# Optimization experiments

Measured on AMD Instinct MI355X. Metric: run time of the kernel, lower is better.

The kernel has to match this reference:

```python
import jax, jax.numpy as jnp
import numpy as np

B, N, IN_DIM, D, H, NC = 4, 1024, 8, 128, 8, 64
DK = D // H      # per-head key/value dim = 16
FF = 512         # hard-coded feedforward hidden
N_ENC = 6        # encoder layers


def _u(key, shape):
    s = 1.0 / np.sqrt(shape[-1])
    return jax.random.uniform(key, shape, jnp.float32, -s, s)


def setup_inputs() -> dict:
    key = jax.random.key(0)
    ks = jax.random.split(key, 24)
    inp = {}
    inp["node_inputs"] = jax.random.normal(ks[0], (B, N, IN_DIM), jnp.float32)
    inp["node_padding_mask"] = jnp.zeros((B, 1, N), jnp.int32)
    inp["edge_mask"] = jax.random.randint(ks[1], (B, N, N), 0, 2).astype(jnp.int32)
    inp["center_mask"] = jnp.zeros((B, 1, NC), jnp.int32)
    inp["center_index"] = jax.random.randint(ks[2], (B, 1, NC), 0, N)
    inp["target_index"] = jax.random.randint(ks[3], (B, 1, 1), 0, N)
    inp["current_index"] = jax.random.randint(ks[4], (B, 1, 1), 0, N)
    inp["edge_inputs"] = jax.random.randint(ks[5], (B, N, 20), 0, N)
    # params
    inp["init_W"] = _u(ks[6], (IN_DIM, D)); inp["init_b"] = jnp.zeros((D,), jnp.float32)
    inp["enc_wq"] = _u(ks[7], (N_ENC, H, D, DK))
    inp["enc_wk"] = _u(ks[8], (N_ENC, H, D, DK))
    inp["enc_wv"] = _u(ks[9], (N_ENC, H, D, DK))
    inp["enc_wo"] = _u(ks[10], (N_ENC, H, DK, D))
    inp["enc_ln1_g"] = jnp.ones((N_ENC, D), jnp.float32); inp["enc_ln1_b"] = jnp.zeros((N_ENC, D), jnp.float32)
    inp["enc_w1"] = _u(ks[11], (N_ENC, D, FF)); inp["enc_b1"] = jnp.zeros((N_ENC, FF), jnp.float32)
    inp["enc_w2"] = _u(ks[12], (N_ENC, FF, D)); inp["enc_b2"] = jnp.zeros((N_ENC, D), jnp.float32)
    inp["enc_ln2_g"] = jnp.ones((N_ENC, D), jnp.float32); inp["enc_ln2_b"] = jnp.zeros((N_ENC, D), jnp.float32)
    inp["dec_wq"] = _u(ks[13], (H, D, DK))
    inp["dec_wk"] = _u(ks[14], (H, D, DK))
    inp["dec_wv"] = _u(ks[15], (H, D, DK))
    inp["dec_wo"] = _u(ks[16], (H, DK, D))
    inp["dec_ln1_g"] = jnp.ones((D,), jnp.float32); inp["dec_ln1_b"] = jnp.zeros((D,), jnp.float32)
    inp["dec_w1"] = _u(ks[17], (D, FF)); inp["dec_b1"] = jnp.zeros((FF,), jnp.float32)
    inp["dec_w2"] = _u(ks[18], (FF, D)); inp["dec_b2"] = jnp.zeros((D,), jnp.float32)
    inp["dec_ln2_g"] = jnp.ones((D,), jnp.float32); inp["dec_ln2_b"] = jnp.zeros((D,), jnp.float32)
    inp["tgt_W"] = _u(ks[19], (2 * D, D)); inp["tgt_b"] = jnp.zeros((D,), jnp.float32)
    inp["ptr_wq"] = _u(ks[20], (D, D))
    inp["ptr_wk"] = _u(ks[21], (D, D))
    return inp


def _ln(x, g, b):
    m = jnp.mean(x, -1, keepdims=True)
    v = jnp.mean((x - m) ** 2, -1, keepdims=True)
    return (x - m) * jax.lax.rsqrt(v + 1e-5) * g + b


def _mha(q, k, v, wq, wk, wv, wo, mask):
    # per-head projections exactly as the torch module: [H, B, n, DK]
    Q = jnp.einsum('bqd,hde->hbqe', q, wq)
    K = jnp.einsum('bkd,hde->hbke', k, wk)
    V = jnp.einsum('bkd,hde->hbke', v, wv)
    U = jnp.einsum('hbqe,hbke->hbqk', Q, K) * (1.0 / np.sqrt(DK))
    if mask is not None:
        U = jnp.where(mask[None] > 0, -1e8, U)
    A = jax.nn.softmax(U, axis=-1)
    Hd = jnp.einsum('hbqk,hbke->hbqe', A, V)
    out = jnp.einsum('hbqe,hed->bqd', Hd, wo)
    return out, A


def _gather(x, idx):
    # x [B, N, D], idx [B, M, 1] -> [B, M, D]  (torch.gather with repeat)
    return jnp.take_along_axis(x, jnp.broadcast_to(idx, (x.shape[0], idx.shape[1], x.shape[2])), axis=1)


def reference(node_inputs, node_padding_mask, edge_mask, center_mask, center_index,
              target_index, current_index, edge_inputs,
              init_W, init_b,
              enc_wq, enc_wk, enc_wv, enc_wo, enc_ln1_g, enc_ln1_b,
              enc_w1, enc_b1, enc_w2, enc_b2, enc_ln2_g, enc_ln2_b,
              dec_wq, dec_wk, dec_wv, dec_wo, dec_ln1_g, dec_ln1_b,
              dec_w1, dec_b1, dec_w2, dec_b2, dec_ln2_g, dec_ln2_b,
              tgt_W, tgt_b, ptr_wq, ptr_wk):
    x = node_inputs @ init_W + init_b                      # initial_embedding
    enc_mask = edge_mask + node_padding_mask               # attn_mask + key_padding_mask, [B,N,N]
    for i in range(N_ENC):                                 # Encoder, 6 layers
        h = _ln(x, enc_ln1_g[i], enc_ln1_b[i])
        a, _ = _mha(h, h, h, enc_wq[i], enc_wk[i], enc_wv[i], enc_wo[i], enc_mask)
        h = a + x
        f = _ln(h, enc_ln2_g[i], enc_ln2_b[i])
        f = jax.nn.relu(f @ enc_w1[i] + enc_b1[i]) @ enc_w2[i] + enc_b2[i]
        x = f + h
    enh = x                                                # enhanced_node_feature [B,N,D]
    ci = jnp.transpose(center_index, (0, 2, 1))            # [B,NC,1]
    tgt_f = _gather(enh, target_index)                     # [B,1,D]
    cur_f = _gather(enh, current_index)                    # [B,1,D]
    cen_f = _gather(enh, ci)                               # [B,NC,D]
    # target_decoder (1 DecoderLayer; normalization1 applied to tgt AND memory)
    tgt_n = _ln(tgt_f, dec_ln1_g, dec_ln1_b)
    mem_n = _ln(enh, dec_ln1_g, dec_ln1_b)
    a, _ = _mha(tgt_n, mem_n, mem_n, dec_wq, dec_wk, dec_wv, dec_wo, node_padding_mask)
    h = a + tgt_f
    f = _ln(h, dec_ln2_g, dec_ln2_b)
    f = jax.nn.relu(f @ dec_w1 + dec_b1) @ dec_w2 + dec_b2
    enh_tgt = f + h                                        # [B,1,D]
    emb_tgt = jnp.concatenate([enh_tgt, tgt_f], -1) @ tgt_W + tgt_b
    # pointer1 (SingleHeadAttention, key_dim = D, tanh clipping 10)
    Q = emb_tgt @ ptr_wq                                   # [B,1,D]
    K = cen_f @ ptr_wk                                     # [B,NC,D]
    U = jnp.einsum('bqd,bkd->bqk', Q, K) * (1.0 / np.sqrt(D))
    U = 10.0 * jnp.tanh(U)
    U = jnp.where(center_mask == 1, -1e8, U)
    center_logp = jax.nn.log_softmax(U, axis=-1)[:, 0, :]  # [B,NC]
    idx = jnp.argmax(center_logp, axis=1)
    bidx = jnp.arange(B)
    selected_center_index = ci[bidx, idx, :]               # [B,1]
    selected_center_feature = cen_f[bidx, idx, :][:, None, :]  # [B,1,D]
    return (enh, cur_f, selected_center_index, selected_center_feature, center_logp, cen_f)
```

## Files before the change

### kernel.cpp

```cpp
#include <hip/hip_runtime.h>

constexpr int kB = 4, kN = 1024, kIn = 8, kD = 128, kH = 8, kNC = 64,
              kDK = 16, kFF = 512, kEnc = 6, kR = kB * kN;

__device__ __forceinline__ float wredsum(float v) {
  v += __shfl_xor(v, 1);  v += __shfl_xor(v, 2);  v += __shfl_xor(v, 4);
  v += __shfl_xor(v, 8);  v += __shfl_xor(v, 16); v += __shfl_xor(v, 32);
  return v;
}
__device__ __forceinline__ float wredmax(float v) {
  v = fmaxf(v, __shfl_xor(v, 1));  v = fmaxf(v, __shfl_xor(v, 2));
  v = fmaxf(v, __shfl_xor(v, 4));  v = fmaxf(v, __shfl_xor(v, 8));
  v = fmaxf(v, __shfl_xor(v, 16)); v = fmaxf(v, __shfl_xor(v, 32));
  return v;
}
__device__ __forceinline__ float red4(float v) {
  v += __shfl_xor(v, 1);  v += __shfl_xor(v, 2);
  return v;
}


__global__ __launch_bounds__(256) void repack_qkv(
    const float* __restrict__ wq, const float* __restrict__ wk,
    const float* __restrict__ wv, float* __restrict__ out, int layers) {
  int i = blockIdx.x * 256 + threadIdx.x;
  if (i >= layers * kD * kD) return;
  int l = i / (kD * kD);
  int rem = i - l * kD * kD;
  int d = rem >> 7;
  int c = rem & 127;
  int src = ((l * kH + (c >> 4)) * kD + d) * kDK + (c & 15);
  out[(size_t)(l * 3 + 0) * 16384 + rem] = wq[src];
  out[(size_t)(l * 3 + 1) * 16384 + rem] = wk[src];
  out[(size_t)(l * 3 + 2) * 16384 + rem] = wv[src];
}

__global__ __launch_bounds__(256) void pack_mask(
    const int* __restrict__ edge_mask, const int* __restrict__ pad_mask,
    unsigned long long* __restrict__ bits_t) {
  int row = blockIdx.x;
  int b = row / kN;
  int q = row % kN;
  int lane = threadIdx.x & 63;
  int wv = threadIdx.x >> 6;
  for (int c0 = wv; c0 < 16; c0 += 4) {
    int k = c0 * 64 + lane;
    int m = edge_mask[(size_t)row * kN + k] + pad_mask[b * kN + k];
    unsigned long long bal = __ballot(m > 0);
    if (lane == 0) bits_t[((size_t)b * 16 + c0) * kN + q] = bal;
  }
}

__global__ __launch_bounds__(256) void pack_pad(
    const int* __restrict__ pad_mask, unsigned long long* __restrict__ bits) {
  int b = blockIdx.x;
  int lane = threadIdx.x & 63;
  int wv = threadIdx.x >> 6;
  for (int c0 = wv; c0 < 16; c0 += 4) {
    int k = c0 * 64 + lane;
    unsigned long long bal = __ballot(pad_mask[b * kN + k] > 0);
    if (lane == 0) bits[b * 16 + c0] = bal;
  }
}

__global__ __launch_bounds__(256) void init_proj(
    const float* __restrict__ ni, const float* __restrict__ W,
    const float* __restrict__ bias, float* __restrict__ x) {
  int i = blockIdx.x * 256 + threadIdx.x;
  int r = i >> 7, c = i & 127;
  float acc = bias[c];
#pragma unroll
  for (int k = 0; k < kIn; k++) acc = fmaf(ni[r * kIn + k], W[k * kD + c], acc);
  x[i] = acc;
}

template <int K, int LN, int RELU, int MODE>
__global__ __launch_bounds__(256) void gtile4(
    const float* __restrict__ A, const float* __restrict__ Wg,
    const float* __restrict__ gamma, const float* __restrict__ beta,
    const float* __restrict__ bias, const float* __restrict__ resid,
    float* __restrict__ O0, float* __restrict__ O1, float* __restrict__ O2,
    int Cfull) {
  constexpr int NC = K / 32;
  __shared__ float As[16][K + 4];
  __shared__ float Ws[2][32][128];
  int r0 = blockIdx.x * 16;
  int y = blockIdx.y;
  const float* Wb;
  int wstride;
  if constexpr (MODE == 2) { Wb = Wg + (size_t)y * K * 128; wstride = 128; }
  else { Wb = Wg + (size_t)y * 128; wstride = Cfull; }

  if constexpr (LN) {
    static_assert(K == 128, "LN requires K==128");
    int w = threadIdx.x >> 6, lane = threadIdx.x & 63;
#pragma unroll
    for (int i = 0; i < 4; i++) {
      int rr = w * 4 + i;
      const float* xr = A + (size_t)(r0 + rr) * 128;
      float2 v = *(const float2*)(xr + lane * 2);
      float mean = wredsum(v.x + v.y) * (1.0f / 128.f);
      float dx = v.x - mean, dy = v.y - mean;
      float var = wredsum(dx * dx + dy * dy) * (1.0f / 128.f);
      float rstd = rsqrtf(var + 1e-5f);
      int c = lane * 2;
      As[rr][c] = dx * rstd * gamma[c] + beta[c];
      As[rr][c + 1] = dy * rstd * gamma[c + 1] + beta[c + 1];
    }
  } else {
    constexpr int NF4 = K / 4;
    for (int f = threadIdx.x; f < 16 * NF4; f += 256) {
      int row = f / NF4, c4i = f % NF4;
      *(float4*)&As[row][c4i * 4] =
          *(const float4*)(A + (size_t)(r0 + row) * K + c4i * 4);
    }
  }

  int wrow = threadIdx.x >> 5;
  int wc4 = threadIdx.x & 31;
  float4 wreg[4];
  auto loadW = [&](int kc) {
    const float* Wr = Wb + (size_t)(kc * 32 + wrow) * wstride + wc4 * 4;
#pragma unroll
    for (int j = 0; j < 4; j++)
      wreg[j] = *(const float4*)(Wr + (size_t)8 * j * wstride);
  };
  auto writeW = [&](int buf) {
#pragma unroll
    for (int j = 0; j < 4; j++)
      *(float4*)&Ws[buf][wrow + 8 * j][wc4 * 4] = wreg[j];
  };

  loadW(0);
  writeW(0);

  int c4 = (threadIdx.x & 31) * 4;
  int rg = threadIdx.x >> 5;
  float acc[2][4] = {};
  for (int kc = 0; kc < NC; kc++) {
    if (kc + 1 < NC) loadW(kc + 1);
    __syncthreads();
#pragma unroll
    for (int k4 = 0; k4 < 8; k4++) {
      float4 a0 = *(const float4*)&As[rg * 2][kc * 32 + k4 * 4];
      float4 a1 = *(const float4*)&As[rg * 2 + 1][kc * 32 + k4 * 4];
#pragma unroll
      for (int m = 0; m < 4; m++) {
        float4 wv = *(const float4*)&Ws[kc & 1][k4 * 4 + m][c4];
        float av0 = ((const float*)&a0)[m];
        float av1 = ((const float*)&a1)[m];
        acc[0][0] = fmaf(av0, wv.x, acc[0][0]);
        acc[0][1] = fmaf(av0, wv.y, acc[0][1]);
        acc[0][2] = fmaf(av0, wv.z, acc[0][2]);
        acc[0][3] = fmaf(av0, wv.w, acc[0][3]);
        acc[1][0] = fmaf(av1, wv.x, acc[1][0]);
        acc[1][1] = fmaf(av1, wv.y, acc[1][1]);
        acc[1][2] = fmaf(av1, wv.z, acc[1][2]);
        acc[1][3] = fmaf(av1, wv.w, acc[1][3]);
      }
    }
    if (kc + 1 < NC) writeW((kc + 1) & 1);
  }

#pragma unroll
  for (int rr = 0; rr < 2; rr++) {
    int r = r0 + rg * 2 + rr;
    if constexpr (MODE == 2) {
#pragma unroll
      for (int j = 0; j < 4; j++) {
        int c = c4 + j;
        float v = acc[rr][j];
        int hh = c >> 4, e = c & 15;
        int bb = r >> 10, n = r & 1023;
        float* P = (y == 0) ? O0 : (y == 1) ? O1 : O2;
        P[(((size_t)(bb * kH + hh)) * kN + n) * kDK + e] = v;
      }
    } else {
      int colg = y * 128 + c4;
      float4 v = make_float4(acc[rr][0], acc[rr][1], acc[rr][2], acc[rr][3]);
      if (bias) {
        float4 bv = *(const float4*)(bias + colg);
        v.x += bv.x; v.y += bv.y; v.z += bv.z; v.w += bv.w;
      }
      if (resid) {
        float4 rv = *(const float4*)(resid + (size_t)r * Cfull + colg);
        v.x += rv.x; v.y += rv.y; v.z += rv.z; v.w += rv.w;
      }
      if (RELU) {
        v.x = fmaxf(v.x, 0.f); v.y = fmaxf(v.y, 0.f);
        v.z = fmaxf(v.z, 0.f); v.w = fmaxf(v.w, 0.f);
      }
      *(float4*)(O0 + (size_t)r * Cfull + colg) = v;
    }
  }
}

__global__ __launch_bounds__(512) void attn_part(
    const float* __restrict__ Q, const float* __restrict__ K,
    const float* __restrict__ V, const unsigned long long* __restrict__ bits_t,
    float* __restrict__ part) {
  __shared__ float Ks[8][64][20];
  __shared__ float Vs[8][64][20];
  int bh = blockIdx.x, qt = blockIdx.y, ks = blockIdx.z;
  int b = bh >> 3;
  int w = threadIdx.x >> 6, lane = threadIdx.x & 63;
  int qbase = qt * 256 + lane;
  float4 qr[4][4];
#pragma unroll
  for (int i = 0; i < 4; i++) {
    const float4* qp = (const float4*)(Q + ((size_t)bh * kN + qbase + i * 64) * kDK);
    qr[i][0] = qp[0]; qr[i][1] = qp[1]; qr[i][2] = qp[2]; qr[i][3] = qp[3];
  }
  int kk = ks * 512 + w * 64 + lane;
  {
    const float4* kp = (const float4*)(K + ((size_t)bh * kN + kk) * kDK);
    const float4* vp = (const float4*)(V + ((size_t)bh * kN + kk) * kDK);
    ((float4*)&Ks[w][lane][0])[0] = kp[0]; ((float4*)&Ks[w][lane][0])[1] = kp[1];
    ((float4*)&Ks[w][lane][0])[2] = kp[2]; ((float4*)&Ks[w][lane][0])[3] = kp[3];
    ((float4*)&Vs[w][lane][0])[0] = vp[0]; ((float4*)&Vs[w][lane][0])[1] = vp[1];
    ((float4*)&Vs[w][lane][0])[2] = vp[2]; ((float4*)&Vs[w][lane][0])[3] = vp[3];
  }
  int tile = ks * 8 + w;
  unsigned long long mb[4];
#pragma unroll
  for (int i = 0; i < 4; i++)
    mb[i] = bits_t[((size_t)b * 16 + tile) * kN + qbase + i * 64];

  float mx[4], lsum[4], acc[4][16];
#pragma unroll
  for (int i = 0; i < 4; i++) {
    mx[i] = -3.0e38f; lsum[i] = 0.f;
#pragma unroll
    for (int e = 0; e < 16; e++) acc[i][e] = 0.f;
  }

#pragma unroll 2
  for (int k2 = 0; k2 < 64; k2++) {
    const float4* kr = (const float4*)&Ks[w][k2][0];
    float4 k0 = kr[0], k1 = kr[1], k2v = kr[2], k3 = kr[3];
    const float4* vr = (const float4*)&Vs[w][k2][0];
    float4 v0 = vr[0], v1 = vr[1], v2 = vr[2], v3 = vr[3];
#pragma unroll
    for (int i = 0; i < 4; i++) {
      float s = qr[i][0].x * k0.x + qr[i][0].y * k0.y + qr[i][0].z * k0.z +
                qr[i][0].w * k0.w + qr[i][1].x * k1.x + qr[i][1].y * k1.y +
                qr[i][1].z * k1.z + qr[i][1].w * k1.w + qr[i][2].x * k2v.x +
                qr[i][2].y * k2v.y + qr[i][2].z * k2v.z + qr[i][2].w * k2v.w +
                qr[i][3].x * k3.x + qr[i][3].y * k3.y + qr[i][3].z * k3.z +
                qr[i][3].w * k3.w;
      s *= 0.25f;
      if ((mb[i] >> k2) & 1ull) s = -1e8f;
      float d = s - mx[i];
      if (d > 8.f) {
        float sc = __expf(-d);
        lsum[i] *= sc;
#pragma unroll
        for (int e = 0; e < 16; e++) acc[i][e] *= sc;
        mx[i] = s; d = 0.f;
      }
      float p = __expf(d);
      lsum[i] += p;
      acc[i][0] = fmaf(p, v0.x, acc[i][0]);
      acc[i][1] = fmaf(p, v0.y, acc[i][1]);
      acc[i][2] = fmaf(p, v0.z, acc[i][2]);
      acc[i][3] = fmaf(p, v0.w, acc[i][3]);
      acc[i][4] = fmaf(p, v1.x, acc[i][4]);
      acc[i][5] = fmaf(p, v1.y, acc[i][5]);
      acc[i][6] = fmaf(p, v1.z, acc[i][6]);
      acc[i][7] = fmaf(p, v1.w, acc[i][7]);
      acc[i][8] = fmaf(p, v2.x, acc[i][8]);
      acc[i][9] = fmaf(p, v2.y, acc[i][9]);
      acc[i][10] = fmaf(p, v2.z, acc[i][10]);
      acc[i][11] = fmaf(p, v2.w, acc[i][11]);
      acc[i][12] = fmaf(p, v3.x, acc[i][12]);
      acc[i][13] = fmaf(p, v3.y, acc[i][13]);
      acc[i][14] = fmaf(p, v3.z, acc[i][14]);
      acc[i][15] = fmaf(p, v3.w, acc[i][15]);
    }
  }
  __syncthreads();
  for (int i = 0; i < 4; i++) {
    float* dst = &Ks[w][lane][0];
#pragma unroll
    for (int e = 0; e < 16; e++) dst[e] = acc[i][e];
    dst[16] = mx[i];
    dst[17] = lsum[i];
    __syncthreads();
    if (w == 0) {
      float mv[8];
#pragma unroll
      for (int p = 0; p < 8; p++) mv[p] = Ks[p][lane][16];
      float mstar = mv[0];
#pragma unroll
      for (int p = 1; p < 8; p++) mstar = fmaxf(mstar, mv[p]);
      float f[8];
      float L = 0.f;
#pragma unroll
      for (int p = 0; p < 8; p++) {
        f[p] = __expf(mv[p] - mstar);
        L += f[p] * Ks[p][lane][17];
      }
      int q = qt * 256 + i * 64 + lane;
      float* op = part + ((size_t)(ks * 32 + bh) * kN + q) * 20;
#pragma unroll
      for (int e = 0; e < 16; e++) {
        float a = 0.f;
#pragma unroll
        for (int p = 0; p < 8; p++) a += f[p] * Ks[p][lane][e];
        op[e] = a;
      }
      op[16] = mstar;
      op[17] = L;
    }
    __syncthreads();
  }
}

__global__ __launch_bounds__(256) void attn_merge(
    const float* __restrict__ part, float* __restrict__ Hd) {
  int idx = blockIdx.x * 256 + threadIdx.x;
  int bh = idx >> 10, q = idx & 1023;
  int b = bh >> 3, h = bh & 7;
  const float* p0 = part + ((size_t)(0 * 32 + bh) * kN + q) * 20;
  const float* p1 = part + ((size_t)(1 * 32 + bh) * kN + q) * 20;
  float m0 = p0[16], l0 = p0[17], m1 = p1[16], l1 = p1[17];
  float ms = fmaxf(m0, m1);
  float f0 = __expf(m0 - ms), f1 = __expf(m1 - ms);
  float inv = 1.0f / (f0 * l0 + f1 * l1);
  float* op = Hd + ((size_t)(b * kN + q)) * kD + h * kDK;
#pragma unroll
  for (int e = 0; e < 16; e++) op[e] = (f0 * p0[e] + f1 * p1[e]) * inv;
}


__global__ __launch_bounds__(256) void dec_prep(
    const float* __restrict__ enh, const int* __restrict__ tgt_idx,
    const int* __restrict__ cur_idx, const int* __restrict__ cen_idx,
    const float* __restrict__ Wq,
    const float* __restrict__ ln1_g, const float* __restrict__ ln1_b,
    const float* __restrict__ dec_wk,
    float* __restrict__ out_curf, float* __restrict__ out_cenf,
    float* __restrict__ tgtf_ws, float* __restrict__ qk_ws) {
  __shared__ float tgtf_s[128], tgtn[128], qd[128];
  int b = blockIdx.x, t = threadIdx.x;
  int lane = t & 63, w = t >> 6;
  int ti = tgt_idx[b], cui = cur_idx[b];
  if (t < 128) {
    float tf = enh[((size_t)b * kN + ti) * kD + t];
    tgtf_s[t] = tf;
    tgtf_ws[b * kD + t] = tf;
    out_curf[b * kD + t] = enh[((size_t)b * kN + cui) * kD + t];
  }
  for (int i = t; i < kNC * kD; i += 256) {
    int c = i >> 7, e = i & 127;
    out_cenf[((size_t)b * kNC + c) * kD + e] =
        enh[((size_t)b * kN + cen_idx[b * kNC + c]) * kD + e];
  }
  __syncthreads();
  if (w == 0) {
    float vx = tgtf_s[lane * 2], vy = tgtf_s[lane * 2 + 1];
    float mean = wredsum(vx + vy) * (1.0f / 128.f);
    float dx = vx - mean, dy = vy - mean;
    float var = wredsum(dx * dx + dy * dy) * (1.0f / 128.f);
    float rstd = rsqrtf(var + 1e-5f);
    tgtn[lane * 2] = dx * rstd * ln1_g[lane * 2] + ln1_b[lane * 2];
    tgtn[lane * 2 + 1] = dy * rstd * ln1_g[lane * 2 + 1] + ln1_b[lane * 2 + 1];
  }
  __syncthreads();
  if (t < 128) {
    float a = 0.f;
#pragma unroll 8
    for (int k = 0; k < 128; k++) a = fmaf(tgtn[k], Wq[k * 128 + t], a);
    qd[t] = a;
  }
  __syncthreads();
  int h = t >> 5, d0 = (t & 31) * 4;
#pragma unroll
  for (int j = 0; j < 4; j++) {
    int d = d0 + j;
    const float4* wp = (const float4*)(dec_wk + (((size_t)h * 128 + d) << 4));
    float a = 0.f;
#pragma unroll
    for (int r = 0; r < 4; r++) {
      float4 wv = wp[r];
      a += wv.x * qd[h * 16 + r * 4] + wv.y * qd[h * 16 + r * 4 + 1] +
           wv.z * qd[h * 16 + r * 4 + 2] + wv.w * qd[h * 16 + r * 4 + 3];
    }
    qk_ws[b * 1024 + h * 128 + d] = 0.25f * a;
  }
}

__global__ __launch_bounds__(256) void dec_score(
    const float* __restrict__ enh, const float* __restrict__ ln_g,
    const float* __restrict__ ln_b, const float* __restrict__ qk_ws,
    const unsigned long long* __restrict__ padbits,
    float* __restrict__ ln_ws, float* __restrict__ scores) {
  __shared__ float qs[8][128];
  int b = blockIdx.x, nt = blockIdx.y, t = threadIdx.x;
  for (int i = t; i < 1024; i += 256) ((float*)qs)[i] = qk_ws[b * 1024 + i];
  __syncthreads();
  int w = t >> 6, lane = t & 63, ri = lane >> 2, q4 = lane & 3;
  int n = nt * 64 + w * 16 + ri;
  const float* row = enh + ((size_t)b * kN + n) * kD;
  float4 xv[8];
#pragma unroll
  for (int j = 0; j < 8; j++) xv[j] = *(const float4*)(row + j * 16 + q4 * 4);
  float s1 = 0.f;
#pragma unroll
  for (int j = 0; j < 8; j++) s1 += xv[j].x + xv[j].y + xv[j].z + xv[j].w;
  s1 = red4(s1);
  float mean = s1 * (1.0f / 128.f);
  float s2 = 0.f;
#pragma unroll
  for (int j = 0; j < 8; j++) {
    xv[j].x -= mean; xv[j].y -= mean; xv[j].z -= mean; xv[j].w -= mean;
    s2 += xv[j].x * xv[j].x + xv[j].y * xv[j].y + xv[j].z * xv[j].z +
          xv[j].w * xv[j].w;
  }
  s2 = red4(s2);
  float rstd = rsqrtf(s2 * (1.0f / 128.f) + 1e-5f);
#pragma unroll
  for (int j = 0; j < 8; j++) {
    int d0 = j * 16 + q4 * 4;
    float4 g = *(const float4*)(ln_g + d0);
    float4 be = *(const float4*)(ln_b + d0);
    xv[j].x = xv[j].x * rstd * g.x + be.x;
    xv[j].y = xv[j].y * rstd * g.y + be.y;
    xv[j].z = xv[j].z * rstd * g.z + be.z;
    xv[j].w = xv[j].w * rstd * g.w + be.w;
    *(float4*)(ln_ws + ((size_t)b * kN + n) * kD + d0) = xv[j];
  }
  bool mk = (padbits[b * 16 + (n >> 6)] >> (n & 63)) & 1ull;
#pragma unroll
  for (int h = 0; h < 8; h++) {
    float p = 0.f;
#pragma unroll
    for (int j = 0; j < 8; j++) {
      float4 qv = *(const float4*)&qs[h][j * 16 + q4 * 4];
      p += xv[j].x * qv.x + xv[j].y * qv.y + xv[j].z * qv.z + xv[j].w * qv.w;
    }
    p = red4(p);
    if (q4 == 0) scores[((size_t)b * 8 + h) * 1024 + n] = mk ? -1e8f : p;
  }
}

__global__ __launch_bounds__(256) void dec_softmax(
    const float* __restrict__ scores, float* __restrict__ ml) {
  int b = blockIdx.x, t = threadIdx.x, w = t >> 6, lane = t & 63;
  for (int hi = 0; hi < 2; hi++) {
    int h = w + hi * 4;
    const float* sr = scores + ((size_t)b * 8 + h) * 1024;
    float v[16];
    float m = -3.0e38f;
#pragma unroll
    for (int i = 0; i < 16; i++) { v[i] = sr[i * 64 + lane]; m = fmaxf(m, v[i]); }
    m = wredmax(m);
    float l = 0.f;
#pragma unroll
    for (int i = 0; i < 16; i++) l += __expf(v[i] - m);
    l = wredsum(l);
    if (lane == 0) { ml[(b * 8 + h) * 2] = m; ml[(b * 8 + h) * 2 + 1] = l; }
  }
}

__global__ __launch_bounds__(256) void dec_attnsum(
    const float* __restrict__ ln_ws, const float* __restrict__ scores,
    const float* __restrict__ ml, float* __restrict__ partial) {
  __shared__ float lns[64][128];
  __shared__ float ps[8][64];
  int b = blockIdx.x, nt = blockIdx.y, t = threadIdx.x;
  for (int i = t; i < 64 * 32; i += 256) {
    int nn = i >> 5, c4 = i & 31;
    *(float4*)&lns[nn][c4 * 4] =
        *(const float4*)(ln_ws + ((size_t)b * kN + nt * 64 + nn) * kD + c4 * 4);
  }
  for (int i = t; i < 512; i += 256) {
    int h = i >> 6, nn = i & 63;
    float m = ml[(b * 8 + h) * 2], l = ml[(b * 8 + h) * 2 + 1];
    ps[h][nn] =
        __expf(scores[((size_t)b * 8 + h) * 1024 + nt * 64 + nn] - m) / l;
  }
  __syncthreads();
  int h = t >> 5, d0 = (t & 31) * 4;
  float4 acc = make_float4(0.f, 0.f, 0.f, 0.f);
  for (int nn = 0; nn < 64; nn++) {
    float p = ps[h][nn];
    float4 lv = *(const float4*)&lns[nn][d0];
    acc.x = fmaf(p, lv.x, acc.x); acc.y = fmaf(p, lv.y, acc.y);
    acc.z = fmaf(p, lv.z, acc.z); acc.w = fmaf(p, lv.w, acc.w);
  }
  *(float4*)(partial + ((size_t)(b * 16 + nt) * 8 + h) * 128 + d0) = acc;
}

__global__ __launch_bounds__(1024) void dec_tail(
    const float* __restrict__ partial, const float* __restrict__ dec_wv,
    const float* __restrict__ dwo, const float* __restrict__ tgtf_ws,
    const float* __restrict__ cenf_g, const float* __restrict__ Kp,
    const int* __restrict__ cen_idx, const int* __restrict__ center_mask,
    const float* __restrict__ ln2_g, const float* __restrict__ ln2_b,
    const float* __restrict__ w1, const float* __restrict__ b1,
    const float* __restrict__ w2, const float* __restrict__ b2,
    const float* __restrict__ tgt_W, const float* __restrict__ tgt_b,
    const float* __restrict__ ptr_wq,
    float* __restrict__ out_selidx, float* __restrict__ out_selfeat,
    float* __restrict__ out_logp) {
  __shared__ float wsum[8][132];
  __shared__ float red[8][132];
  __shared__ float red2[2][520];
  __shared__ float red16[16][68];
  __shared__ float tgtf[128], hdd[128], dechs[128], decfs[128], dects[512],
                   embs[128], qps[128];
  __shared__ int bi_s;
  int b = blockIdx.x, t = threadIdx.x;
  int c = t & 127, p = t >> 7;
  int lane = t & 63, w = t >> 6;

  {
    float a = 0.f;
#pragma unroll
    for (int tt = 0; tt < 16; tt++)
      a += partial[((size_t)(b * 16 + tt) * 8 + p) * 128 + c];
    wsum[p][c] = a;
    if (t < 128) tgtf[t] = tgtf_ws[b * kD + t];
  }
  __syncthreads();

  {
    int h = c >> 4, e = c & 15;
    float a = 0.f;
#pragma unroll
    for (int i = 0; i < 16; i++) {
      int d = p * 16 + i;
      a = fmaf(wsum[h][d], dec_wv[((size_t)h * 128 + d) * 16 + e], a);
    }
    red[p][c] = a;
  }
  __syncthreads();
  if (t < 128) {
    float a = 0.f;
#pragma unroll
    for (int q = 0; q < 8; q++) a += red[q][t];
    hdd[t] = a;
  }
  __syncthreads();

  {
    float a = 0.f;
#pragma unroll
    for (int i = 0; i < 16; i++) {
      int k = p * 16 + i;
      a = fmaf(hdd[k], dwo[k * 128 + c], a);
    }
    red[p][c] = a;
  }
  __syncthreads();
  if (t < 128) {
    float a = 0.f;
#pragma unroll
    for (int q = 0; q < 8; q++) a += red[q][t];
    dechs[t] = a + tgtf[t];
  }
  __syncthreads();

  if (w == 0) {
    float vx = dechs[lane * 2], vy = dechs[lane * 2 + 1];
    float mean = wredsum(vx + vy) * (1.0f / 128.f);
    float dx = vx - mean, dy = vy - mean;
    float var = wredsum(dx * dx + dy * dy) * (1.0f / 128.f);
    float rstd = rsqrtf(var + 1e-5f);
    decfs[lane * 2] = dx * rstd * ln2_g[lane * 2] + ln2_b[lane * 2];
    decfs[lane * 2 + 1] = dy * rstd * ln2_g[lane * 2 + 1] + ln2_b[lane * 2 + 1];
  }
  __syncthreads();

  {
    int c5 = t & 511, p2 = t >> 9;
    float a = 0.f;
#pragma unroll 8
    for (int i = 0; i < 64; i++) {
      int k = p2 * 64 + i;
      a = fmaf(decfs[k], w1[k * 512 + c5], a);
    }
    red2[p2][c5] = a;
  }
  __syncthreads();
  if (t < 512) dects[t] = fmaxf(red2[0][t] + red2[1][t] + b1[t], 0.f);
  __syncthreads();

  {
    float a = 0.f;
#pragma unroll 8
    for (int i = 0; i < 64; i++) {
      int k = p * 64 + i;
      a = fmaf(dects[k], w2[k * 128 + c], a);
    }
    red[p][c] = a;
  }
  __syncthreads();
  if (t < 128) {
    float a = 0.f;
#pragma unroll
    for (int q = 0; q < 8; q++) a += red[q][t];
    decfs[t] = a + b2[t] + dechs[t];
  }
  __syncthreads();

  {
    float a = 0.f;
#pragma unroll
    for (int i = 0; i < 32; i++) {
      int k = p * 32 + i;
      float vkk = (k < 128) ? decfs[k] : tgtf[k - 128];
      a = fmaf(vkk, tgt_W[k * 128 + c], a);
    }
    red[p][c] = a;
  }
  __syncthreads();
  if (t < 128) {
    float a = 0.f;
#pragma unroll
    for (int q = 0; q < 8; q++) a += red[q][t];
    embs[t] = a + tgt_b[t];
  }
  __syncthreads();

  {
    float a = 0.f;
#pragma unroll
    for (int i = 0; i < 16; i++) {
      int k = p * 16 + i;
      a = fmaf(embs[k], ptr_wq[k * 128 + c], a);
    }
    red[p][c] = a;
  }
  __syncthreads();
  if (t < 128) {
    float a = 0.f;
#pragma unroll
    for (int q = 0; q < 8; q++) a += red[q][t];
    qps[t] = a;
  }
  __syncthreads();

  {
    int cen = t & 63, p16 = t >> 6;
    float a = 0.f;
#pragma unroll
    for (int i = 0; i < 8; i++) {
      int k = p16 * 8 + i;
      a = fmaf(qps[k], Kp[((size_t)(b * kNC + cen)) * kD + k], a);
    }
    red16[p16][cen] = a;
  }
  __syncthreads();
  if (w == 0) {
    float u = 0.f;
#pragma unroll
    for (int q = 0; q < 16; q++) u += red16[q][lane];
    u *= 0.08838834764831845f;
    u = 10.0f * tanhf(u);
    if (center_mask[b * kNC + lane] == 1) u = -1e8f;
    float m = wredmax(u);
    float ex = __expf(u - m);
    float sum = wredsum(ex);
    out_logp[b * kNC + lane] = u - m - logf(sum);
    float bm = u; int bi = lane;
#pragma unroll
    for (int o = 32; o; o >>= 1) {
      float om = __shfl_xor(bm, o);
      int oi = __shfl_xor(bi, o);
      if (om > bm || (om == bm && oi < bi)) { bm = om; bi = oi; }
    }
    if (lane == 0) {
      out_selidx[b] = (float)cen_idx[b * kNC + bi];
      bi_s = bi;
    }
  }
  __syncthreads();
  if (t < 128)
    out_selfeat[b * kD + t] = cenf_g[((size_t)(b * kNC + bi_s)) * kD + t];
}


extern "C" void kernel_launch(void* const* d_in, const int* in_sizes, int n_in,
                              void* d_out, int out_size, void* d_ws,
                              size_t ws_size, hipStream_t stream) {
  (void)in_sizes; (void)n_in; (void)out_size; (void)ws_size;
  const float* node_inputs = (const float*)d_in[0];
  const int* pad_mask = (const int*)d_in[1];
  const int* edge_mask = (const int*)d_in[2];
  const int* center_mask = (const int*)d_in[3];
  const int* center_index = (const int*)d_in[4];
  const int* target_index = (const int*)d_in[5];
  const int* current_index = (const int*)d_in[6];
  const float* init_W = (const float*)d_in[8];
  const float* init_b = (const float*)d_in[9];
  const float* enc_wq = (const float*)d_in[10];
  const float* enc_wk = (const float*)d_in[11];
  const float* enc_wv = (const float*)d_in[12];
  const float* enc_wo = (const float*)d_in[13];
  const float* enc_ln1_g = (const float*)d_in[14];
  const float* enc_ln1_b = (const float*)d_in[15];
  const float* enc_w1 = (const float*)d_in[16];
  const float* enc_b1 = (const float*)d_in[17];
  const float* enc_w2 = (const float*)d_in[18];
  const float* enc_b2 = (const float*)d_in[19];
  const float* enc_ln2_g = (const float*)d_in[20];
  const float* enc_ln2_b = (const float*)d_in[21];
  const float* dec_wq = (const float*)d_in[22];
  const float* dec_wk = (const float*)d_in[23];
  const float* dec_wv = (const float*)d_in[24];
  const float* dec_wo = (const float*)d_in[25];
  const float* dec_ln1_g = (const float*)d_in[26];
  const float* dec_ln1_b = (const float*)d_in[27];
  const float* dec_w1 = (const float*)d_in[28];
  const float* dec_b1 = (const float*)d_in[29];
  const float* dec_w2 = (const float*)d_in[30];
  const float* dec_b2 = (const float*)d_in[31];
  const float* dec_ln2_g = (const float*)d_in[32];
  const float* dec_ln2_b = (const float*)d_in[33];
  const float* tgt_W = (const float*)d_in[34];
  const float* tgt_b = (const float*)d_in[35];
  const float* ptr_wq = (const float*)d_in[36];
  const float* ptr_wk = (const float*)d_in[37];

  float* out_enh = (float*)d_out;
  float* out_curf = out_enh + kB * kN * kD;
  float* out_selidx = out_curf + kB * kD;
  float* out_selfeat = out_selidx + kB;
  float* out_logp = out_selfeat + kB * kD;
  float* out_cenf = out_logp + kB * kNC;

  char* wsp = (char*)d_ws;
  size_t off = 0;
  auto alloc = [&](size_t n) {
    char* p = wsp + off;
    off = (off + n + 255) & ~(size_t)255;
    return p;
  };
  float* x   = (float*)alloc(kR * kD * 4);
  float* h2  = (float*)alloc(kR * kD * 4);
  float* Qb  = (float*)alloc(kR * kD * 4);
  float* Kb  = (float*)alloc(kR * kD * 4);
  float* Vb  = (float*)alloc(kR * kD * 4);
  float* Hd  = (float*)alloc(kR * kD * 4);
  float* tb  = (float*)alloc(kR * kFF * 4);
  unsigned long long* bits_t  = (unsigned long long*)alloc(kR * 16 * 8);
  unsigned long long* padbits = (unsigned long long*)alloc(kB * 16 * 8);
  float* ewqkv = (float*)alloc(kEnc * 3 * kD * kD * 4);
  float* dqkvW = (float*)alloc(3 * kD * kD * 4);
  float* ln_ws = (float*)alloc(kR * kD * 4);
  float* scores_ws = (float*)alloc(kB * kH * kN * 4);
  float* ml_ws = (float*)alloc(kB * kH * 2 * 4);
  float* partial_ws = (float*)alloc(kB * 16 * kH * kD * 4);
  float* qk_ws = (float*)alloc(kB * kH * kD * 4);
  float* tgtf_ws = (float*)alloc(kB * kD * 4);
  float* Kp_ws = (float*)alloc(kB * kNC * kD * 4);
  float* apart_ws = (float*)alloc((size_t)2 * 32 * kN * 20 * 4);

  repack_qkv<<<(kEnc * kD * kD + 255) / 256, 256, 0, stream>>>(
      enc_wq, enc_wk, enc_wv, ewqkv, kEnc);
  repack_qkv<<<(kD * kD + 255) / 256, 256, 0, stream>>>(
      dec_wq, dec_wk, dec_wv, dqkvW, 1);
  pack_mask<<<kB * kN, 256, 0, stream>>>(edge_mask, pad_mask, bits_t);
  pack_pad<<<kB, 256, 0, stream>>>(pad_mask, padbits);
  init_proj<<<kR * kD / 256, 256, 0, stream>>>(node_inputs, init_W, init_b, x);

  for (int l = 0; l < kEnc; l++) {
    const float* wo_l = enc_wo + (size_t)l * kH * kDK * kD;
    gtile4<128, 1, 0, 2><<<dim3(kR / 16, 3), 256, 0, stream>>>(
        x, ewqkv + (size_t)l * 3 * kD * kD, enc_ln1_g + l * kD,
        enc_ln1_b + l * kD, nullptr, nullptr, Qb, Kb, Vb, kD);
    attn_part<<<dim3(kB * kH, kN / 256, 2), 512, 0, stream>>>(Qb, Kb, Vb,
                                                              bits_t, apart_ws);
    attn_merge<<<(kB * kH * kN) / 256, 256, 0, stream>>>(apart_ws, Hd);
    gtile4<128, 0, 0, 0><<<dim3(kR / 16, 1), 256, 0, stream>>>(
        Hd, wo_l, nullptr, nullptr, nullptr, x, h2, nullptr, nullptr, kD);
    gtile4<128, 1, 1, 0><<<dim3(kR / 16, kFF / 128), 256, 0, stream>>>(
        h2, enc_w1 + (size_t)l * kD * kFF, enc_ln2_g + l * kD,
        enc_ln2_b + l * kD, enc_b1 + l * kFF, nullptr, tb, nullptr, nullptr, kFF);
    float* xout = (l == kEnc - 1) ? out_enh : x;
    gtile4<512, 0, 0, 0><<<dim3(kR / 16, 1), 256, 0, stream>>>(
        tb, enc_w2 + (size_t)l * kFF * kD, nullptr, nullptr, enc_b2 + l * kD,
        h2, xout, nullptr, nullptr, kD);
  }

  dec_prep<<<kB, 256, 0, stream>>>(out_enh, target_index, current_index,
                                   center_index, dqkvW, dec_ln1_g, dec_ln1_b,
                                   dec_wk, out_curf, out_cenf, tgtf_ws, qk_ws);
  gtile4<128, 0, 0, 0><<<dim3(kB * kNC / 16, 1), 256, 0, stream>>>(
      out_cenf, ptr_wk, nullptr, nullptr, nullptr, nullptr, Kp_ws, nullptr,
      nullptr, kD);
  dec_score<<<dim3(kB, 16), 256, 0, stream>>>(out_enh, dec_ln1_g, dec_ln1_b,
                                              qk_ws, padbits, ln_ws, scores_ws);
  dec_softmax<<<kB, 256, 0, stream>>>(scores_ws, ml_ws);
  dec_attnsum<<<dim3(kB, 16), 256, 0, stream>>>(ln_ws, scores_ws, ml_ws,
                                                partial_ws);
  dec_tail<<<kB, 1024, 0, stream>>>(
      partial_ws, dec_wv, dec_wo, tgtf_ws, out_cenf, Kp_ws, center_index,
      center_mask, dec_ln2_g, dec_ln2_b, dec_w1, dec_b1, dec_w2, dec_b2,
      tgt_W, tgt_b, ptr_wq, out_selidx, out_selfeat, out_logp);
}
```

Before: 824.6 us.

## Fuse attention split-merge into output projection GEMM and shrink attn LDS

Removes the separate attn_merge kernel and the Hd buffer by adding a MODE 3 A-loader to gtile4 that merges the two key-split partial softmax results directly while staging the A tile. Separately, attn_part now stages K/V through shared memory in two 32-row halves, roughly halving its LDS footprint so more blocks can be resident. This saves one launch per layer and a full write and read of the head output, at the cost of a heavier A-load in the projection GEMM with strided partial reads. The scratch reuse during the final reduction still fits the smaller buffer.

```diff
diff --git a/kernel.cpp b/kernel.cpp
--- a/kernel.cpp
+++ b/kernel.cpp
@@ -106,6 +106,28 @@
       int c = lane * 2;
       As[rr][c] = dx * rstd * gamma[c] + beta[c];
       As[rr][c + 1] = dy * rstd * gamma[c + 1] + beta[c + 1];
+    }
+  } else if constexpr (MODE == 3) {
+    static_assert(K == 128, "merge stage requires K==128");
+    for (int f = threadIdx.x; f < 16 * 32; f += 256) {
+      int row = f >> 5, c4i = f & 31;
+      int r = r0 + row;
+      int bb = r >> 10, q = r & 1023;
+      int hh = c4i >> 2, e4 = (c4i & 3) * 4;
+      const float* p0 = A + ((size_t)((bb * kH + hh) * kN + q)) * 20;
+      const float* p1 = p0 + (size_t)32 * kN * 20;
+      float m0 = p0[16], l0 = p0[17], m1 = p1[16], l1 = p1[17];
+      float ms = fmaxf(m0, m1);
+      float f0 = __expf(m0 - ms), f1 = __expf(m1 - ms);
+      float inv = 1.0f / (f0 * l0 + f1 * l1);
+      float4 a0 = *(const float4*)(p0 + e4);
+      float4 a1 = *(const float4*)(p1 + e4);
+      float4 o;
+      o.x = (f0 * a0.x + f1 * a1.x) * inv;
+      o.y = (f0 * a0.y + f1 * a1.y) * inv;
+      o.z = (f0 * a0.z + f1 * a1.z) * inv;
+      o.w = (f0 * a0.w + f1 * a1.w) * inv;
+      *(float4*)&As[row][c4i * 4] = o;
     }
   } else {
     constexpr int NF4 = K / 4;
@@ -199,8 +221,7 @@
     const float* __restrict__ Q, const float* __restrict__ K,
     const float* __restrict__ V, const unsigned long long* __restrict__ bits_t,
     float* __restrict__ part) {
-  __shared__ float Ks[8][64][20];
-  __shared__ float Vs[8][64][20];
+  __shared__ float KV[2][8][32][20];
   int bh = blockIdx.x, qt = blockIdx.y, ks = blockIdx.z;
   int b = bh >> 3;
   int w = threadIdx.x >> 6, lane = threadIdx.x & 63;
@@ -208,17 +229,9 @@
   float4 qr[4][4];
 #pragma unroll
   for (int i = 0; i < 4; i++) {
-    const float4* qp = (const float4*)(Q + ((size_t)bh * kN + qbase + i * 64) * kDK);
+    const float4* qp =
+        (const float4*)(Q + ((size_t)bh * kN + qbase + i * 64) * kDK);
     qr[i][0] = qp[0]; qr[i][1] = qp[1]; qr[i][2] = qp[2]; qr[i][3] = qp[3];
-  }
-  int kk = ks * 512 + w * 64 + lane;
-  {
-    const float4* kp = (const float4*)(K + ((size_t)bh * kN + kk) * kDK);
-    const float4* vp = (const float4*)(V + ((size_t)bh * kN + kk) * kDK);
-    ((float4*)&Ks[w][lane][0])[0] = kp[0]; ((float4*)&Ks[w][lane][0])[1] = kp[1];
-    ((float4*)&Ks[w][lane][0])[2] = kp[2]; ((float4*)&Ks[w][lane][0])[3] = kp[3];
-    ((float4*)&Vs[w][lane][0])[0] = vp[0]; ((float4*)&Vs[w][lane][0])[1] = vp[1];
-    ((float4*)&Vs[w][lane][0])[2] = vp[2]; ((float4*)&Vs[w][lane][0])[3] = vp[3];
   }
   int tile = ks * 8 + w;
   unsigned long long mb[4];
@@ -234,53 +247,67 @@
     for (int e = 0; e < 16; e++) acc[i][e] = 0.f;
   }
 
+  int srow = lane >> 1, shalf = (lane & 1) * 8;
+  for (int st = 0; st < 2; st++) {
+    int kb = ks * 512 + w * 64 + st * 32;
+    {
+      const float* kr = K + ((size_t)bh * kN + kb + srow) * kDK + shalf;
+      const float* vr = V + ((size_t)bh * kN + kb + srow) * kDK + shalf;
+      *(float4*)&KV[0][w][srow][shalf] = *(const float4*)kr;
+      *(float4*)&KV[0][w][srow][shalf + 4] = *(const float4*)(kr + 4);
+      *(float4*)&KV[1][w][srow][shalf] = *(const float4*)vr;
+      *(float4*)&KV[1][w][srow][shalf + 4] = *(const float4*)(vr + 4);
+    }
 #pragma unroll 2
-  for (int k2 = 0; k2 < 64; k2++) {
-    const float4* kr = (const float4*)&Ks[w][k2][0];
-    float4 k0 = kr[0], k1 = kr[1], k2v = kr[2], k3 = kr[3];
-    const float4* vr = (const float4*)&Vs[w][k2][0];
-    float4 v0 = vr[0], v1 = vr[1], v2 = vr[2], v3 = vr[3];
-#pragma unroll
-    for (int i = 0; i < 4; i++) {
-      float s = qr[i][0].x * k0.x + qr[i][0].y * k0.y + qr[i][0].z * k0.z +
-                qr[i][0].w * k0.w + qr[i][1].x * k1.x + qr[i][1].y * k1.y +
-                qr[i][1].z * k1.z + qr[i][1].w * k1.w + qr[i][2].x * k2v.x +
-                qr[i][2].y * k2v.y + qr[i][2].z * k2v.z + qr[i][2].w * k2v.w +
-                qr[i][3].x * k3.x + qr[i][3].y * k3.y + qr[i][3].z * k3.z +
-                qr[i][3].w * k3.w;
-      s *= 0.25f;
-      if ((mb[i] >> k2) & 1ull) s = -1e8f;
-      float d = s - mx[i];
-      if (d > 8.f) {
-        float sc = __expf(-d);
-        lsum[i] *= sc;
-#pragma unroll
-        for (int e = 0; e < 16; e++) acc[i][e] *= sc;
-        mx[i] = s; d = 0.f;
+    for (int k2 = 0; k2 < 32; k2++) {
+      const float4* kr4 = (const float4*)&KV[0][w][k2][0];
+      float4 k0 = kr4[0], k1 = kr4[1], k2v = kr4[2], k3 = kr4[3];
+      const float4* vr4 = (const float4*)&KV[1][w][k2][0];
+      float4 v0 = vr4[0], v1 = vr4[1], v2 = vr4[2], v3 = vr4[3];
+      int kbit = st * 32 + k2;
+#pragma unroll
+      for (int i = 0; i < 4; i++) {
+        float s = qr[i][0].x * k0.x + qr[i][0].y * k0.y + qr[i][0].z * k0.z +
+                  qr[i][0].w * k0.w + qr[i][1].x * k1.x + qr[i][1].y * k1.y +
+                  qr[i][1].z * k1.z + qr[i][1].w * k1.w + qr[i][2].x * k2v.x +
+                  qr[i][2].y * k2v.y + qr[i][2].z * k2v.z + qr[i][2].w * k2v.w +
+                  qr[i][3].x * k3.x + qr[i][3].y * k3.y + qr[i][3].z * k3.z +
+                  qr[i][3].w * k3.w;
+        s *= 0.25f;
+        if ((mb[i] >> kbit) & 1ull) s = -1e8f;
+        float d = s - mx[i];
+        if (d > 8.f) {
+          float sc = __expf(-d);
+          lsum[i] *= sc;
+#pragma unroll
+          for (int e = 0; e < 16; e++) acc[i][e] *= sc;
+          mx[i] = s; d = 0.f;
+        }
+        float p = __expf(d);
+        lsum[i] += p;
+        acc[i][0] = fmaf(p, v0.x, acc[i][0]);
+        acc[i][1] = fmaf(p, v0.y, acc[i][1]);
+        acc[i][2] = fmaf(p, v0.z, acc[i][2]);
+        acc[i][3] = fmaf(p, v0.w, acc[i][3]);
+        acc[i][4] = fmaf(p, v1.x, acc[i][4]);
+        acc[i][5] = fmaf(p, v1.y, acc[i][5]);
+        acc[i][6] = fmaf(p, v1.z, acc[i][6]);
+        acc[i][7] = fmaf(p, v1.w, acc[i][7]);
+        acc[i][8] = fmaf(p, v2.x, acc[i][8]);
+        acc[i][9] = fmaf(p, v2.y, acc[i][9]);
+        acc[i][10] = fmaf(p, v2.z, acc[i][10]);
+        acc[i][11] = fmaf(p, v2.w, acc[i][11]);
+        acc[i][12] = fmaf(p, v3.x, acc[i][12]);
+        acc[i][13] = fmaf(p, v3.y, acc[i][13]);
+        acc[i][14] = fmaf(p, v3.z, acc[i][14]);
+        acc[i][15] = fmaf(p, v3.w, acc[i][15]);
       }
-      float p = __expf(d);
-      lsum[i] += p;
-      acc[i][0] = fmaf(p, v0.x, acc[i][0]);
-      acc[i][1] = fmaf(p, v0.y, acc[i][1]);
-      acc[i][2] = fmaf(p, v0.z, acc[i][2]);
-      acc[i][3] = fmaf(p, v0.w, acc[i][3]);
-      acc[i][4] = fmaf(p, v1.x, acc[i][4]);
-      acc[i][5] = fmaf(p, v1.y, acc[i][5]);
-      acc[i][6] = fmaf(p, v1.z, acc[i][6]);
-      acc[i][7] = fmaf(p, v1.w, acc[i][7]);
-      acc[i][8] = fmaf(p, v2.x, acc[i][8]);
-      acc[i][9] = fmaf(p, v2.y, acc[i][9]);
-      acc[i][10] = fmaf(p, v2.z, acc[i][10]);
-      acc[i][11] = fmaf(p, v2.w, acc[i][11]);
-      acc[i][12] = fmaf(p, v3.x, acc[i][12]);
-      acc[i][13] = fmaf(p, v3.y, acc[i][13]);
-      acc[i][14] = fmaf(p, v3.z, acc[i][14]);
-      acc[i][15] = fmaf(p, v3.w, acc[i][15]);
-    }
-  }
-  __syncthreads();
+    }
+  }
+  __syncthreads();
+  float* scratch = &KV[0][0][0][0];
   for (int i = 0; i < 4; i++) {
-    float* dst = &Ks[w][lane][0];
+    float* dst = scratch + (size_t)(w * 64 + lane) * 20;
 #pragma unroll
     for (int e = 0; e < 16; e++) dst[e] = acc[i][e];
     dst[16] = mx[i];
@@ -289,7 +316,7 @@
     if (w == 0) {
       float mv[8];
 #pragma unroll
-      for (int p = 0; p < 8; p++) mv[p] = Ks[p][lane][16];
+      for (int p = 0; p < 8; p++) mv[p] = scratch[(p * 64 + lane) * 20 + 16];
       float mstar = mv[0];
 #pragma unroll
       for (int p = 1; p < 8; p++) mstar = fmaxf(mstar, mv[p]);
@@ -298,7 +325,7 @@
 #pragma unroll
       for (int p = 0; p < 8; p++) {
         f[p] = __expf(mv[p] - mstar);
-        L += f[p] * Ks[p][lane][17];
+        L += f[p] * scratch[(p * 64 + lane) * 20 + 17];
       }
       int q = qt * 256 + i * 64 + lane;
       float* op = part + ((size_t)(ks * 32 + bh) * kN + q) * 20;
@@ -306,7 +333,7 @@
       for (int e = 0; e < 16; e++) {
         float a = 0.f;
 #pragma unroll
-        for (int p = 0; p < 8; p++) a += f[p] * Ks[p][lane][e];
+        for (int p = 0; p < 8; p++) a += f[p] * scratch[(p * 64 + lane) * 20 + e];
         op[e] = a;
       }
       op[16] = mstar;
@@ -314,22 +341,6 @@
     }
     __syncthreads();
   }
-}
-
-__global__ __launch_bounds__(256) void attn_merge(
-    const float* __restrict__ part, float* __restrict__ Hd) {
-  int idx = blockIdx.x * 256 + threadIdx.x;
-  int bh = idx >> 10, q = idx & 1023;
-  int b = bh >> 3, h = bh & 7;
-  const float* p0 = part + ((size_t)(0 * 32 + bh) * kN + q) * 20;
-  const float* p1 = part + ((size_t)(1 * 32 + bh) * kN + q) * 20;
-  float m0 = p0[16], l0 = p0[17], m1 = p1[16], l1 = p1[17];
-  float ms = fmaxf(m0, m1);
-  float f0 = __expf(m0 - ms), f1 = __expf(m1 - ms);
-  float inv = 1.0f / (f0 * l0 + f1 * l1);
-  float* op = Hd + ((size_t)(b * kN + q)) * kD + h * kDK;
-#pragma unroll
-  for (int e = 0; e < 16; e++) op[e] = (f0 * p0[e] + f1 * p1[e]) * inv;
 }
 
 
@@ -743,7 +754,6 @@
   float* Qb  = (float*)alloc(kR * kD * 4);
   float* Kb  = (float*)alloc(kR * kD * 4);
   float* Vb  = (float*)alloc(kR * kD * 4);
-  float* Hd  = (float*)alloc(kR * kD * 4);
   float* tb  = (float*)alloc(kR * kFF * 4);
   unsigned long long* bits_t  = (unsigned long long*)alloc(kR * 16 * 8);
   unsigned long long* padbits = (unsigned long long*)alloc(kB * 16 * 8);
@@ -773,9 +783,8 @@
         enc_ln1_b + l * kD, nullptr, nullptr, Qb, Kb, Vb, kD);
     attn_part<<<dim3(kB * kH, kN / 256, 2), 512, 0, stream>>>(Qb, Kb, Vb,
                                                               bits_t, apart_ws);
-    attn_merge<<<(kB * kH * kN) / 256, 256, 0, stream>>>(apart_ws, Hd);
-    gtile4<128, 0, 0, 0><<<dim3(kR / 16, 1), 256, 0, stream>>>(
-        Hd, wo_l, nullptr, nullptr, nullptr, x, h2, nullptr, nullptr, kD);
+    gtile4<128, 0, 0, 3><<<dim3(kR / 16, 1), 256, 0, stream>>>(
+        apart_ws, wo_l, nullptr, nullptr, nullptr, x, h2, nullptr, nullptr, kD);
     gtile4<128, 1, 1, 0><<<dim3(kR / 16, kFF / 128), 256, 0, stream>>>(
         h2, enc_w1 + (size_t)l * kD * kFF, enc_ln2_g + l * kD,
         enc_ln2_b + l * kD, enc_b1 + l * kFF, nullptr, tb, nullptr, nullptr, kFF);
```

After: 814.2 us. No clear change (-1.3%).
